# Optimization experiments

Hardware: AMD Instinct MI355X
Metric: run time of the kernel (lower is better)

The kernel has to match this reference:

```python
import jax, jax.numpy as jnp
import numpy as np

# Synthetic forest: T complete B-ary trees of depth D.
# Nodes stored level-major in `embeds`: level 0 (roots) first, then level 1, ...
# Level l has T*B**l nodes; children of node j at level l are rows j*B..j*B+B-1 of level l+1.
T_TREES, BRANCH, DEPTH = 16, 4, 8
IN_DIM, HIDDEN, N_LABEL = 128, 128, 5


def _level_layout():
    counts = [T_TREES * BRANCH ** l for l in range(DEPTH)]
    offsets = np.concatenate([[0], np.cumsum(counts)]).astype(np.int64)
    return counts, offsets


def setup_inputs() -> dict:
    key = jax.random.key(0)
    counts, offsets = _level_layout()
    n_total = int(offsets[-1])
    ks = jax.random.split(key, 16)
    s_in = 1.0 / np.sqrt(IN_DIM)
    s_h = 1.0 / np.sqrt(HIDDEN)
    d = {"embeds": jax.random.normal(ks[0], (n_total, IN_DIM), dtype=jnp.float32)}
    # gate params: *x linears have bias, *h linears are bias-free (as in torch module)
    d["Wix"] = jax.random.uniform(ks[1], (HIDDEN, IN_DIM), jnp.float32, -s_in, s_in)
    d["bix"] = jax.random.uniform(ks[2], (HIDDEN,), jnp.float32, -s_in, s_in)
    d["Wih"] = jax.random.uniform(ks[3], (HIDDEN, HIDDEN), jnp.float32, -s_h, s_h)
    d["Wfx"] = jax.random.uniform(ks[4], (HIDDEN, IN_DIM), jnp.float32, -s_in, s_in)
    d["bfx"] = jax.random.uniform(ks[5], (HIDDEN,), jnp.float32, -s_in, s_in)
    d["Wfh"] = jax.random.uniform(ks[6], (HIDDEN, HIDDEN), jnp.float32, -s_h, s_h)
    d["Wox"] = jax.random.uniform(ks[7], (HIDDEN, IN_DIM), jnp.float32, -s_in, s_in)
    d["box"] = jax.random.uniform(ks[8], (HIDDEN,), jnp.float32, -s_in, s_in)
    d["Woh"] = jax.random.uniform(ks[9], (HIDDEN, HIDDEN), jnp.float32, -s_h, s_h)
    d["Wux"] = jax.random.uniform(ks[10], (HIDDEN, IN_DIM), jnp.float32, -s_in, s_in)
    d["bux"] = jax.random.uniform(ks[11], (HIDDEN,), jnp.float32, -s_in, s_in)
    d["Wuh"] = jax.random.uniform(ks[12], (HIDDEN, HIDDEN), jnp.float32, -s_h, s_h)
    d["Wout"] = 0.01 * jax.random.normal(ks[13], (N_LABEL, HIDDEN), dtype=jnp.float32)
    d["bout"] = 0.01 * jax.random.normal(ks[14], (N_LABEL,), dtype=jnp.float32)
    return d


def reference(embeds, Wix, bix, Wih, Wfx, bfx, Wfh, Wox, box, Woh, Wux, bux, Wuh, Wout, bout):
    counts, offsets = _level_layout()
    H, B = HIDDEN, BRANCH
    child_h = child_c = None
    # leaves-first (level = DEPTH-1 .. 0), matching `while level >= 0` order
    for level in range(DEPTH - 1, -1, -1):
        n = counts[level]
        o = int(offsets[level])
        x = embeds[o:o + n]  # [n, in_dim] == index_select of this level's nodes
        if child_h is None:  # leaves: zero child state
            h_sum = jnp.zeros((n, H), embeds.dtype)
            fc_sum = jnp.zeros((n, H), embeds.dtype)
        else:
            # child-sum over the B children gathered from the previous level
            h_sum = child_h.reshape(n, B, H).sum(axis=1)  # child_h_sum
            fh = child_h @ Wfh.T  # [n*B, H]
            fx = jnp.repeat(x, B, axis=0) @ Wfx.T + bfx  # parent embed per child
            f = jax.nn.sigmoid(fx + fh)
            fc_sum = (f * child_c).reshape(n, B, H).sum(axis=1)  # child_fc_sum
        i = jax.nn.sigmoid(x @ Wix.T + bix + h_sum @ Wih.T)
        og = jax.nn.sigmoid(x @ Wox.T + box + h_sum @ Woh.T)
        u = jnp.tanh(x @ Wux.T + bux + h_sum @ Wuh.T)
        c = i * u + fc_sum
        h = og * jnp.tanh(c)
        child_c, child_h = c, h
    # output head at the root level (dropout is identity at eval)
    return child_h @ Wout.T + bout  # [T_TREES, N_LABEL]
```

## Files before the change

### kernel.cpp

```cpp
#include <hip/hip_runtime.h>
#include <hip/hip_bf16.h>


#define HID 128

typedef unsigned short u16;
typedef unsigned int u32;
typedef __attribute__((ext_vector_type(8))) short short8;
typedef __attribute__((ext_vector_type(4))) float floatx4;

__device__ __forceinline__ float bf2f(u16 u) {
  union { unsigned int u; float f; } v; v.u = ((unsigned int)u) << 16; return v.f;
}
__device__ __forceinline__ u16 f2bf(float f) {
  __hip_bfloat16 b = __float2bfloat16(f);
  return *reinterpret_cast<u16*>(&b);
}
__device__ __forceinline__ short8 f2bf8(float4 f0, float4 f1) {
  short8 s;
  s[0] = (short)f2bf(f0.x); s[1] = (short)f2bf(f0.y);
  s[2] = (short)f2bf(f0.z); s[3] = (short)f2bf(f0.w);
  s[4] = (short)f2bf(f1.x); s[5] = (short)f2bf(f1.y);
  s[6] = (short)f2bf(f1.z); s[7] = (short)f2bf(f1.w);
  return s;
}
__device__ __forceinline__ float sigm(float x) {
  return __builtin_amdgcn_rcpf(1.0f + __expf(-x));
}
__device__ __forceinline__ float tanh_fast(float x) {
  float ax = fabsf(x);
  float e = __expf(2.0f * ax);
  float t = 1.0f - 2.0f * __builtin_amdgcn_rcpf(e + 1.0f);
  return copysignf(t, x);
}

__global__ void prep_weights(const float* __restrict__ Wix, const float* __restrict__ Wih,
                             const float* __restrict__ Wfx, const float* __restrict__ Wfh,
                             const float* __restrict__ Wox, const float* __restrict__ Woh,
                             const float* __restrict__ Wux, const float* __restrict__ Wuh,
                             u16* __restrict__ Wcat, u16* __restrict__ Wfxb, u16* __restrict__ Wfhb)
{
  int t = blockIdx.x * 256 + threadIdx.x;
  if (t < 98304) {
    int nrow = t >> 8, k = t & 255;
    int gate = nrow >> 7, r = nrow & 127;
    float v;
    if (k < 128) {
      const float* W = (gate == 0) ? Wix : (gate == 1) ? Wox : Wux;
      v = W[r * 128 + k];
    } else {
      const float* W = (gate == 0) ? Wih : (gate == 1) ? Woh : Wuh;
      v = W[r * 128 + (k - 128)];
    }
    Wcat[t] = f2bf(v);
  } else if (t < 98304 + 16384) {
    int i = t - 98304;
    Wfxb[i] = f2bf(Wfx[i]);
  } else if (t < 98304 + 32768) {
    int i = t - 98304 - 16384;
    Wfhb[i] = f2bf(Wfh[i]);
  }
}

template <int MODE>
__global__ __launch_bounds__(512, 2)
void tree_kernel(const float* __restrict__ embeds,
                 const u16* __restrict__ Wcat,
                 const u16* __restrict__ Wfxb,
                 const u16* __restrict__ Wfhb,
                 const float* __restrict__ bix, const float* __restrict__ bfx,
                 const float* __restrict__ box, const float* __restrict__ bux,
                 u16* __restrict__ hf, float* __restrict__ fc_buf,
                 int n, int noff, int poff)
{
  constexpr bool HASC = (MODE >= 1);
  constexpr bool HASP = (MODE != 2);
  constexpr int OFF_SHS  = 16384;
  constexpr int OFF_SXP  = OFF_SHS + (HASC ? 16384 : 0);
  constexpr int OFF_SFXP = OFF_SXP + (HASP ? 4096 : 0);
  constexpr int SMEM_SZ  = OFF_SFXP + (HASP ? 16 * 132 * 4 : 0);
  __shared__ char smem[SMEM_SZ];
  u16*   sx   = (u16*)smem;
  u16*   shs  = (u16*)(smem + OFF_SHS);
  u16*   sxp  = (u16*)(smem + OFF_SXP);
  float* sfxp = (float*)(smem + OFF_SFXP);

  const int tid  = threadIdx.x;
  const int wave = tid >> 6;
  const int lane = tid & 63;
  const int lg   = lane >> 4;
  const int ln   = lane & 15;
  const int pbase = blockIdx.x * 64;
  const int col  = wave * 16 + ln;

  {
    int row = tid >> 3;
    int k0  = (tid & 7) * 16;
    const float* src = embeds + (size_t)(noff + pbase + row) * HID + k0;
    unsigned sw = ((unsigned)(row & 7)) << 4;
    char* dst = (char*)sx + row * 256;
    float4 f0 = *(const float4*)src;
    float4 f1 = *(const float4*)(src + 4);
    float4 f2 = *(const float4*)(src + 8);
    float4 f3 = *(const float4*)(src + 12);
    *(short8*)(dst + (((unsigned)(k0 * 2)) ^ sw))      = f2bf8(f0, f1);
    *(short8*)(dst + (((unsigned)(k0 * 2 + 16)) ^ sw)) = f2bf8(f2, f3);
  }
  if constexpr (HASC) {
    int row = tid >> 3, cg = tid & 7;
    const u16* src = hf + (size_t)(noff + pbase + row) * HID + cg * 16;
    short8 v0 = *(const short8*)src;
    short8 v1 = *(const short8*)(src + 8);
    unsigned sw = ((unsigned)(row & 7)) << 4;
    char* dst = (char*)shs + row * 256;
    *(short8*)(dst + ((cg * 32) ^ sw))      = v0;
    *(short8*)(dst + ((cg * 32 + 16) ^ sw)) = v1;
  }
  if constexpr (HASP) {
    if (tid < 128) {
      int row = tid >> 3;
      int k0  = (tid & 7) * 16;
      const float* src = embeds + (size_t)(poff + (pbase >> 2) + row) * HID + k0;
      unsigned sw = ((unsigned)(row & 7)) << 4;
      char* dst = (char*)sxp + row * 256;
      float4 f0 = *(const float4*)src;
      float4 f1 = *(const float4*)(src + 4);
      float4 f2 = *(const float4*)(src + 8);
      float4 f3 = *(const float4*)(src + 12);
      *(short8*)(dst + (((unsigned)(k0 * 2)) ^ sw))      = f2bf8(f0, f1);
      *(short8*)(dst + (((unsigned)(k0 * 2 + 16)) ^ sw)) = f2bf8(f2, f3);
    }
  }
  __syncthreads();

  float fcown[4][4];
  if constexpr (HASC) {
#pragma unroll
    for (int m = 0; m < 4; ++m)
#pragma unroll
      for (int r = 0; r < 4; ++r)
        fcown[m][r] = fc_buf[(size_t)(noff + pbase + m * 16 + lg * 4 + r) * HID + col];
  }

  floatx4 acc[4][3] = {};
  constexpr int KT = HASC ? 8 : 4;
#pragma unroll
  for (int kt = 0; kt < KT; ++kt) {
    short8 a[4];
#pragma unroll
    for (int m = 0; m < 4; ++m) {
      int row = m * 16 + ln;
      unsigned sw = ((unsigned)(row & 7)) << 4;
      const char* base = (kt < 4) ? (const char*)sx : (const char*)shs;
      int kb = ((kt & 3) * 32 + lg * 8) * 2;
      a[m] = *(const short8*)(base + row * 256 + (((unsigned)kb) ^ sw));
    }
#pragma unroll
    for (int g = 0; g < 3; ++g) {
      short8 b = *(const short8*)(Wcat + (size_t)((g * 8 + wave) * 16 + ln) * 256 + kt * 32 + lg * 8);
#pragma unroll
      for (int m = 0; m < 4; ++m)
        acc[m][g] = __builtin_amdgcn_mfma_f32_16x16x32_bf16(a[m], b, acc[m][g], 0, 0, 0);
    }
  }

  if constexpr (HASP) {
    floatx4 accxp = {};
#pragma unroll
    for (int kt = 0; kt < 4; ++kt) {
      short8 b = *(const short8*)(Wfxb + (size_t)(wave * 16 + ln) * HID + kt * 32 + lg * 8);
      unsigned sw = ((unsigned)(ln & 7)) << 4;
      short8 a = *(const short8*)((char*)sxp + ln * 256 +
                                  (((unsigned)((kt * 32 + lg * 8) * 2)) ^ sw));
      accxp = __builtin_amdgcn_mfma_f32_16x16x32_bf16(a, b, accxp, 0, 0, 0);
    }
#pragma unroll
    for (int r = 0; r < 4; ++r)
      sfxp[(lg * 4 + r) * 132 + col] = accxp[r];
  }
  __syncthreads();

  float cv[4][4];
  {
    float bi = bix[col], bo = box[col], bu = bux[col];
#pragma unroll
    for (int m = 0; m < 4; ++m) {
      float hs4 = 0.f;
#pragma unroll
      for (int r = 0; r < 4; ++r) {
        int row = m * 16 + lg * 4 + r;
        bool ok = (MODE == 2) ? (pbase + row < n) : true;
        if (ok) {
          float iv = sigm(acc[m][0][r] + bi);
          float ov = sigm(acc[m][1][r] + bo);
          float uv = tanh_fast(acc[m][2][r] + bu);
          float fcv = HASC ? fcown[m][r] : 0.f;
          float c = iv * uv + fcv;
          float hv = ov * tanh_fast(c);
          if constexpr (MODE == 2) {
            hf[(size_t)(noff + pbase + row) * HID + col] = f2bf(hv);
          } else {
            cv[m][r] = c;
            hs4 += hv;
            unsigned sw = ((unsigned)(row & 7)) << 4;
            *(u16*)((char*)sx + row * 256 + (((unsigned)(col * 2)) ^ sw)) = f2bf(hv);
          }
        }
      }
      if constexpr (HASP)
        hf[(size_t)(poff + (pbase >> 2) + m * 4 + lg) * HID + col] = f2bf(hs4);
    }
  }

  if constexpr (HASP) {
    __syncthreads();
    floatx4 ah[4] = {};
#pragma unroll
    for (int kt = 0; kt < 4; ++kt) {
      short8 b = *(const short8*)(Wfhb + (size_t)(wave * 16 + ln) * HID + kt * 32 + lg * 8);
#pragma unroll
      for (int m = 0; m < 4; ++m) {
        int row = m * 16 + ln;
        unsigned sw = ((unsigned)(row & 7)) << 4;
        short8 a = *(const short8*)((char*)sx + row * 256 +
                                    (((unsigned)((kt * 32 + lg * 8) * 2)) ^ sw));
        ah[m] = __builtin_amdgcn_mfma_f32_16x16x32_bf16(a, b, ah[m], 0, 0, 0);
      }
    }
    float bf = bfx[col];
#pragma unroll
    for (int m = 0; m < 4; ++m) {
      float fxv = sfxp[(m * 4 + lg) * 132 + col] + bf;
      float s = 0.f;
#pragma unroll
      for (int r = 0; r < 4; ++r)
        s += sigm(fxv + ah[m][r]) * cv[m][r];
      fc_buf[(size_t)(poff + (pbase >> 2) + m * 4 + lg) * HID + col] = s;
    }
  }
}

__global__ void out_kernel(const u16* __restrict__ hf, const float* __restrict__ Wout,
                           const float* __restrict__ bout, float* __restrict__ out)
{
  int t = threadIdx.x;
  if (t < 80) {
    int row = t / 5, lbl = t - row * 5;
    float s = bout[lbl];
    for (int k = 0; k < 128; ++k)
      s += bf2f(hf[row * 128 + k]) * Wout[lbl * 128 + k];
    out[t] = s;
  }
}

extern "C" void kernel_launch(void* const* d_in, const int* in_sizes, int n_in,
                              void* d_out, int out_size, void* d_ws, size_t ws_size,
                              hipStream_t stream)
{
  const float* embeds = (const float*)d_in[0];
  const float* Wix = (const float*)d_in[1];
  const float* bix = (const float*)d_in[2];
  const float* Wih = (const float*)d_in[3];
  const float* Wfx = (const float*)d_in[4];
  const float* bfx = (const float*)d_in[5];
  const float* Wfh = (const float*)d_in[6];
  const float* Wox = (const float*)d_in[7];
  const float* box = (const float*)d_in[8];
  const float* Woh = (const float*)d_in[9];
  const float* Wux = (const float*)d_in[10];
  const float* bux = (const float*)d_in[11];
  const float* Wuh = (const float*)d_in[12];
  const float* Wout = (const float*)d_in[13];
  const float* bout = (const float*)d_in[14];

  static const int counts[8]  = {16, 64, 256, 1024, 4096, 16384, 65536, 262144};
  static const int offsets[9] = {0, 16, 80, 336, 1360, 5456, 21840, 87376, 349520};

  char* ws = (char*)d_ws;
  u16*   hf     = (u16*)ws;
  float* fc_buf = (float*)(ws + 89477120);
  u16*   Wcat   = (u16*)(ws + 89477120 + 178954240);
  u16*   Wfxb   = Wcat + 384 * 256;
  u16*   Wfhb   = Wfxb + 128 * 128;

  prep_weights<<<512, 256, 0, stream>>>(Wix, Wih, Wfx, Wfh, Wox, Woh, Wux, Wuh,
                                        Wcat, Wfxb, Wfhb);

  tree_kernel<0><<<262144 / 64, 512, 0, stream>>>(
      embeds, Wcat, Wfxb, Wfhb, bix, bfx, box, bux,
      hf, fc_buf, 262144, 87376, 21840);

  for (int l = 6; l >= 1; --l) {
    int nl = counts[l];
    tree_kernel<1><<<nl / 64, 512, 0, stream>>>(
        embeds, Wcat, Wfxb, Wfhb, bix, bfx, box, bux,
        hf, fc_buf, nl, offsets[l], offsets[l - 1]);
  }

  tree_kernel<2><<<1, 512, 0, stream>>>(
      embeds, Wcat, Wfxb, Wfhb, bix, bfx, box, bux,
      hf, fc_buf, 16, 0, 0);

  out_kernel<<<1, 128, 0, stream>>>(hf, Wout, bout, (float*)d_out);
}
```

Before: 247.4 us.

## Fuse top tree levels and output head into one kernel; read parent embeds directly

Levels 2, 1 and 0 plus the output projection now run in a single persistent kernel with 4 blocks, each owning 4 root subtrees and looping over levels in shared memory. This removes four small kernel launches and their inter-kernel gaps. Separately, the parent-embedding forget-gate GEMM now reads fp32 embeds straight from global memory into MFMA operands instead of staging them in shared memory, which saves LDS space and a staging step. The fused tail uses only 4 blocks, so its per-level work is serialized within each block.

```diff
diff --git a/kernel.cpp b/kernel.cpp
--- a/kernel.cpp
+++ b/kernel.cpp
@@ -71,18 +71,15 @@
                  const float* __restrict__ bix, const float* __restrict__ bfx,
                  const float* __restrict__ box, const float* __restrict__ bux,
                  u16* __restrict__ hf, float* __restrict__ fc_buf,
-                 int n, int noff, int poff)
+                 int noff, int poff)
 {
   constexpr bool HASC = (MODE >= 1);
-  constexpr bool HASP = (MODE != 2);
   constexpr int OFF_SHS  = 16384;
-  constexpr int OFF_SXP  = OFF_SHS + (HASC ? 16384 : 0);
-  constexpr int OFF_SFXP = OFF_SXP + (HASP ? 4096 : 0);
-  constexpr int SMEM_SZ  = OFF_SFXP + (HASP ? 16 * 132 * 4 : 0);
+  constexpr int OFF_SFXP = OFF_SHS + (HASC ? 16384 : 0);
+  constexpr int SMEM_SZ  = OFF_SFXP + 16 * 132 * 4;
   __shared__ char smem[SMEM_SZ];
   u16*   sx   = (u16*)smem;
   u16*   shs  = (u16*)(smem + OFF_SHS);
-  u16*   sxp  = (u16*)(smem + OFF_SXP);
   float* sfxp = (float*)(smem + OFF_SFXP);
 
   const int tid  = threadIdx.x;
@@ -92,6 +89,7 @@
   const int ln   = lane & 15;
   const int pbase = blockIdx.x * 64;
   const int col  = wave * 16 + ln;
+  const int prow0 = poff + (pbase >> 2);
 
   {
     int row = tid >> 3;
@@ -116,13 +114,146 @@
     *(short8*)(dst + ((cg * 32) ^ sw))      = v0;
     *(short8*)(dst + ((cg * 32 + 16) ^ sw)) = v1;
   }
-  if constexpr (HASP) {
-    if (tid < 128) {
+  __syncthreads();
+
+  float fcown[4][4];
+  if constexpr (HASC) {
+#pragma unroll
+    for (int m = 0; m < 4; ++m)
+#pragma unroll
+      for (int r = 0; r < 4; ++r)
+        fcown[m][r] = fc_buf[(size_t)(noff + pbase + m * 16 + lg * 4 + r) * HID + col];
+  }
+
+  floatx4 acc[4][3] = {};
+  constexpr int KT = HASC ? 8 : 4;
+#pragma unroll
+  for (int kt = 0; kt < KT; ++kt) {
+    short8 a[4];
+#pragma unroll
+    for (int m = 0; m < 4; ++m) {
+      int row = m * 16 + ln;
+      unsigned sw = ((unsigned)(row & 7)) << 4;
+      const char* base = (kt < 4) ? (const char*)sx : (const char*)shs;
+      int kb = ((kt & 3) * 32 + lg * 8) * 2;
+      a[m] = *(const short8*)(base + row * 256 + (((unsigned)kb) ^ sw));
+    }
+#pragma unroll
+    for (int g = 0; g < 3; ++g) {
+      short8 b = *(const short8*)(Wcat + (size_t)((g * 8 + wave) * 16 + ln) * 256 + kt * 32 + lg * 8);
+#pragma unroll
+      for (int m = 0; m < 4; ++m)
+        acc[m][g] = __builtin_amdgcn_mfma_f32_16x16x32_bf16(a[m], b, acc[m][g], 0, 0, 0);
+    }
+  }
+
+  {
+    floatx4 accxp = {};
+    const float* xprow = embeds + (size_t)(prow0 + ln) * HID;
+#pragma unroll
+    for (int kt = 0; kt < 4; ++kt) {
+      short8 b = *(const short8*)(Wfxb + (size_t)(wave * 16 + ln) * HID + kt * 32 + lg * 8);
+      float4 f0 = *(const float4*)(xprow + kt * 32 + lg * 8);
+      float4 f1 = *(const float4*)(xprow + kt * 32 + lg * 8 + 4);
+      accxp = __builtin_amdgcn_mfma_f32_16x16x32_bf16(f2bf8(f0, f1), b, accxp, 0, 0, 0);
+    }
+#pragma unroll
+    for (int r = 0; r < 4; ++r)
+      sfxp[(lg * 4 + r) * 132 + col] = accxp[r];
+  }
+  __syncthreads();
+
+  float cv[4][4];
+  {
+    float bi = bix[col], bo = box[col], bu = bux[col];
+#pragma unroll
+    for (int m = 0; m < 4; ++m) {
+      float hs4 = 0.f;
+#pragma unroll
+      for (int r = 0; r < 4; ++r) {
+        int row = m * 16 + lg * 4 + r;
+        float iv = sigm(acc[m][0][r] + bi);
+        float ov = sigm(acc[m][1][r] + bo);
+        float uv = tanh_fast(acc[m][2][r] + bu);
+        float fcv = HASC ? fcown[m][r] : 0.f;
+        float c = iv * uv + fcv;
+        float hv = ov * tanh_fast(c);
+        cv[m][r] = c;
+        hs4 += hv;
+        unsigned sw = ((unsigned)(row & 7)) << 4;
+        *(u16*)((char*)sx + row * 256 + (((unsigned)(col * 2)) ^ sw)) = f2bf(hv);
+      }
+      hf[(size_t)(prow0 + m * 4 + lg) * HID + col] = f2bf(hs4);
+    }
+  }
+
+  {
+    __syncthreads();
+    floatx4 ah[4] = {};
+#pragma unroll
+    for (int kt = 0; kt < 4; ++kt) {
+      short8 b = *(const short8*)(Wfhb + (size_t)(wave * 16 + ln) * HID + kt * 32 + lg * 8);
+#pragma unroll
+      for (int m = 0; m < 4; ++m) {
+        int row = m * 16 + ln;
+        unsigned sw = ((unsigned)(row & 7)) << 4;
+        short8 a = *(const short8*)((char*)sx + row * 256 +
+                                    (((unsigned)((kt * 32 + lg * 8) * 2)) ^ sw));
+        ah[m] = __builtin_amdgcn_mfma_f32_16x16x32_bf16(a, b, ah[m], 0, 0, 0);
+      }
+    }
+    float bf = bfx[col];
+#pragma unroll
+    for (int m = 0; m < 4; ++m) {
+      float fxv = sfxp[(m * 4 + lg) * 132 + col] + bf;
+      float s = 0.f;
+#pragma unroll
+      for (int r = 0; r < 4; ++r)
+        s += sigm(fxv + ah[m][r]) * cv[m][r];
+      fc_buf[(size_t)(prow0 + m * 4 + lg) * HID + col] = s;
+    }
+  }
+}
+
+__global__ __launch_bounds__(512, 2)
+void fused_tail(const float* __restrict__ embeds,
+                const u16* __restrict__ Wcat,
+                const u16* __restrict__ Wfxb,
+                const u16* __restrict__ Wfhb,
+                const float* __restrict__ bix, const float* __restrict__ bfx,
+                const float* __restrict__ box, const float* __restrict__ bux,
+                const float* __restrict__ Wout, const float* __restrict__ bout,
+                u16* __restrict__ hf, float* __restrict__ fc_buf,
+                float* __restrict__ out)
+{
+  __shared__ char smem[16384 + 16384 + 16 * 132 * 4];
+  u16*   sx   = (u16*)smem;
+  u16*   shs  = (u16*)(smem + 16384);
+  float* sfxp = (float*)(smem + 32768);
+
+  const int tid  = threadIdx.x;
+  const int wave = tid >> 6;
+  const int lane = tid & 63;
+  const int lg   = lane >> 4;
+  const int ln   = lane & 15;
+  const int col  = wave * 16 + ln;
+  const int b    = blockIdx.x;
+
+  const int offs[3] = {0, 16, 80};
+
+#pragma unroll 1
+  for (int l = 2; l >= 0; --l) {
+    const int nrows = 64 >> (2 * (2 - l));
+    const int noff  = offs[l] + b * nrows;
+    const bool last = (l == 0);
+    const int poff  = last ? 0 : offs[l - 1] + b * (nrows >> 2);
+
+    {
       int row = tid >> 3;
       int k0  = (tid & 7) * 16;
-      const float* src = embeds + (size_t)(poff + (pbase >> 2) + row) * HID + k0;
+      const float* src = embeds + (size_t)(noff + row) * HID + k0;
       unsigned sw = ((unsigned)(row & 7)) << 4;
-      char* dst = (char*)sxp + row * 256;
+      char* dst = (char*)sx + row * 256;
       float4 f0 = *(const float4*)src;
       float4 f1 = *(const float4*)(src + 4);
       float4 f2 = *(const float4*)(src + 8);
@@ -130,126 +261,129 @@
       *(short8*)(dst + (((unsigned)(k0 * 2)) ^ sw))      = f2bf8(f0, f1);
       *(short8*)(dst + (((unsigned)(k0 * 2 + 16)) ^ sw)) = f2bf8(f2, f3);
     }
-  }
-  __syncthreads();
-
-  float fcown[4][4];
-  if constexpr (HASC) {
+    {
+      int row = tid >> 3, cg = tid & 7;
+      const u16* src = hf + (size_t)(noff + row) * HID + cg * 16;
+      short8 v0 = *(const short8*)src;
+      short8 v1 = *(const short8*)(src + 8);
+      unsigned sw = ((unsigned)(row & 7)) << 4;
+      char* dst = (char*)shs + row * 256;
+      *(short8*)(dst + ((cg * 32) ^ sw))      = v0;
+      *(short8*)(dst + ((cg * 32 + 16) ^ sw)) = v1;
+    }
+    __syncthreads();
+
+    float fcown[4][4];
 #pragma unroll
     for (int m = 0; m < 4; ++m)
 #pragma unroll
       for (int r = 0; r < 4; ++r)
-        fcown[m][r] = fc_buf[(size_t)(noff + pbase + m * 16 + lg * 4 + r) * HID + col];
-  }
-
-  floatx4 acc[4][3] = {};
-  constexpr int KT = HASC ? 8 : 4;
-#pragma unroll
-  for (int kt = 0; kt < KT; ++kt) {
-    short8 a[4];
-#pragma unroll
-    for (int m = 0; m < 4; ++m) {
-      int row = m * 16 + ln;
-      unsigned sw = ((unsigned)(row & 7)) << 4;
-      const char* base = (kt < 4) ? (const char*)sx : (const char*)shs;
-      int kb = ((kt & 3) * 32 + lg * 8) * 2;
-      a[m] = *(const short8*)(base + row * 256 + (((unsigned)kb) ^ sw));
-    }
-#pragma unroll
-    for (int g = 0; g < 3; ++g) {
-      short8 b = *(const short8*)(Wcat + (size_t)((g * 8 + wave) * 16 + ln) * 256 + kt * 32 + lg * 8);
-#pragma unroll
-      for (int m = 0; m < 4; ++m)
-        acc[m][g] = __builtin_amdgcn_mfma_f32_16x16x32_bf16(a[m], b, acc[m][g], 0, 0, 0);
-    }
-  }
-
-  if constexpr (HASP) {
-    floatx4 accxp = {};
-#pragma unroll
-    for (int kt = 0; kt < 4; ++kt) {
-      short8 b = *(const short8*)(Wfxb + (size_t)(wave * 16 + ln) * HID + kt * 32 + lg * 8);
-      unsigned sw = ((unsigned)(ln & 7)) << 4;
-      short8 a = *(const short8*)((char*)sxp + ln * 256 +
-                                  (((unsigned)((kt * 32 + lg * 8) * 2)) ^ sw));
-      accxp = __builtin_amdgcn_mfma_f32_16x16x32_bf16(a, b, accxp, 0, 0, 0);
-    }
-#pragma unroll
-    for (int r = 0; r < 4; ++r)
-      sfxp[(lg * 4 + r) * 132 + col] = accxp[r];
-  }
-  __syncthreads();
-
-  float cv[4][4];
-  {
-    float bi = bix[col], bo = box[col], bu = bux[col];
-#pragma unroll
-    for (int m = 0; m < 4; ++m) {
-      float hs4 = 0.f;
-#pragma unroll
-      for (int r = 0; r < 4; ++r) {
-        int row = m * 16 + lg * 4 + r;
-        bool ok = (MODE == 2) ? (pbase + row < n) : true;
-        if (ok) {
-          float iv = sigm(acc[m][0][r] + bi);
-          float ov = sigm(acc[m][1][r] + bo);
-          float uv = tanh_fast(acc[m][2][r] + bu);
-          float fcv = HASC ? fcown[m][r] : 0.f;
-          float c = iv * uv + fcv;
-          float hv = ov * tanh_fast(c);
-          if constexpr (MODE == 2) {
-            hf[(size_t)(noff + pbase + row) * HID + col] = f2bf(hv);
-          } else {
+        fcown[m][r] = fc_buf[(size_t)(noff + m * 16 + lg * 4 + r) * HID + col];
+
+    floatx4 acc[4][3] = {};
+#pragma unroll
+    for (int kt = 0; kt < 8; ++kt) {
+      short8 a[4];
+#pragma unroll
+      for (int m = 0; m < 4; ++m) {
+        int row = m * 16 + ln;
+        unsigned sw = ((unsigned)(row & 7)) << 4;
+        const char* base = (kt < 4) ? (const char*)sx : (const char*)shs;
+        int kb = ((kt & 3) * 32 + lg * 8) * 2;
+        a[m] = *(const short8*)(base + row * 256 + (((unsigned)kb) ^ sw));
+      }
+#pragma unroll
+      for (int g = 0; g < 3; ++g) {
+        short8 bb = *(const short8*)(Wcat + (size_t)((g * 8 + wave) * 16 + ln) * 256 + kt * 32 + lg * 8);
+#pragma unroll
+        for (int m = 0; m < 4; ++m)
+          acc[m][g] = __builtin_amdgcn_mfma_f32_16x16x32_bf16(a[m], bb, acc[m][g], 0, 0, 0);
+      }
+    }
+
+    if (!last) {
+      floatx4 accxp = {};
+      const float* xprow = embeds + (size_t)(poff + ln) * HID;
+#pragma unroll
+      for (int kt = 0; kt < 4; ++kt) {
+        short8 bb = *(const short8*)(Wfxb + (size_t)(wave * 16 + ln) * HID + kt * 32 + lg * 8);
+        float4 f0 = *(const float4*)(xprow + kt * 32 + lg * 8);
+        float4 f1 = *(const float4*)(xprow + kt * 32 + lg * 8 + 4);
+        accxp = __builtin_amdgcn_mfma_f32_16x16x32_bf16(f2bf8(f0, f1), bb, accxp, 0, 0, 0);
+      }
+#pragma unroll
+      for (int r = 0; r < 4; ++r)
+        sfxp[(lg * 4 + r) * 132 + col] = accxp[r];
+    }
+    __syncthreads();
+
+    float cv[4][4];
+    {
+      float bi = bix[col], bo = box[col], bu = bux[col];
+#pragma unroll
+      for (int m = 0; m < 4; ++m) {
+        float hs4 = 0.f;
+#pragma unroll
+        for (int r = 0; r < 4; ++r) {
+          int row = m * 16 + lg * 4 + r;
+          if (row < nrows) {
+            float iv = sigm(acc[m][0][r] + bi);
+            float ov = sigm(acc[m][1][r] + bo);
+            float uv = tanh_fast(acc[m][2][r] + bu);
+            float c = iv * uv + fcown[m][r];
+            float hv = ov * tanh_fast(c);
             cv[m][r] = c;
             hs4 += hv;
             unsigned sw = ((unsigned)(row & 7)) << 4;
             *(u16*)((char*)sx + row * 256 + (((unsigned)(col * 2)) ^ sw)) = f2bf(hv);
           }
         }
-      }
-      if constexpr (HASP)
-        hf[(size_t)(poff + (pbase >> 2) + m * 4 + lg) * HID + col] = f2bf(hs4);
-    }
-  }
-
-  if constexpr (HASP) {
+        if (!last && (m * 4 + lg) < (nrows >> 2))
+          hf[(size_t)(poff + m * 4 + lg) * HID + col] = f2bf(hs4);
+      }
+    }
+
+    if (!last) {
+      __syncthreads();
+      floatx4 ah[4] = {};
+#pragma unroll
+      for (int kt = 0; kt < 4; ++kt) {
+        short8 bb = *(const short8*)(Wfhb + (size_t)(wave * 16 + ln) * HID + kt * 32 + lg * 8);
+#pragma unroll
+        for (int m = 0; m < 4; ++m) {
+          int row = m * 16 + ln;
+          unsigned sw = ((unsigned)(row & 7)) << 4;
+          short8 a = *(const short8*)((char*)sx + row * 256 +
+                                      (((unsigned)((kt * 32 + lg * 8) * 2)) ^ sw));
+          ah[m] = __builtin_amdgcn_mfma_f32_16x16x32_bf16(a, bb, ah[m], 0, 0, 0);
+        }
+      }
+      float bf = bfx[col];
+#pragma unroll
+      for (int m = 0; m < 4; ++m) {
+        if ((m * 4 + lg) < (nrows >> 2)) {
+          float fxv = sfxp[(m * 4 + lg) * 132 + col] + bf;
+          float s = 0.f;
+#pragma unroll
+          for (int r = 0; r < 4; ++r)
+            s += sigm(fxv + ah[m][r]) * cv[m][r];
+          fc_buf[(size_t)(poff + m * 4 + lg) * HID + col] = s;
+        }
+      }
+    }
     __syncthreads();
-    floatx4 ah[4] = {};
-#pragma unroll
-    for (int kt = 0; kt < 4; ++kt) {
-      short8 b = *(const short8*)(Wfhb + (size_t)(wave * 16 + ln) * HID + kt * 32 + lg * 8);
-#pragma unroll
-      for (int m = 0; m < 4; ++m) {
-        int row = m * 16 + ln;
-        unsigned sw = ((unsigned)(row & 7)) << 4;
-        short8 a = *(const short8*)((char*)sx + row * 256 +
-                                    (((unsigned)((kt * 32 + lg * 8) * 2)) ^ sw));
-        ah[m] = __builtin_amdgcn_mfma_f32_16x16x32_bf16(a, b, ah[m], 0, 0, 0);
-      }
-    }
-    float bf = bfx[col];
-#pragma unroll
-    for (int m = 0; m < 4; ++m) {
-      float fxv = sfxp[(m * 4 + lg) * 132 + col] + bf;
-      float s = 0.f;
-#pragma unroll
-      for (int r = 0; r < 4; ++r)
-        s += sigm(fxv + ah[m][r]) * cv[m][r];
-      fc_buf[(size_t)(poff + (pbase >> 2) + m * 4 + lg) * HID + col] = s;
-    }
-  }
-}
-
-__global__ void out_kernel(const u16* __restrict__ hf, const float* __restrict__ Wout,
-                           const float* __restrict__ bout, float* __restrict__ out)
-{
-  int t = threadIdx.x;
-  if (t < 80) {
-    int row = t / 5, lbl = t - row * 5;
+  }
+
+  if (tid < 20) {
+    int r = tid / 5, lbl = tid - r * 5;
+    unsigned sw = ((unsigned)r) << 4;
     float s = bout[lbl];
+    const float* wr = Wout + lbl * 128;
+    const char* hrow = (const char*)sx + r * 256;
+#pragma unroll 4
     for (int k = 0; k < 128; ++k)
-      s += bf2f(hf[row * 128 + k]) * Wout[lbl * 128 + k];
-    out[t] = s;
+      s += bf2f(*(const u16*)(hrow + (((unsigned)(k * 2)) ^ sw))) * wr[k];
+    out[(4 * b + r) * 5 + lbl] = s;
   }
 }
 
@@ -288,18 +422,16 @@
 
   tree_kernel<0><<<262144 / 64, 512, 0, stream>>>(
       embeds, Wcat, Wfxb, Wfhb, bix, bfx, box, bux,
-      hf, fc_buf, 262144, 87376, 21840);
-
-  for (int l = 6; l >= 1; --l) {
+      hf, fc_buf, 87376, 21840);
+
+  for (int l = 6; l >= 3; --l) {
     int nl = counts[l];
     tree_kernel<1><<<nl / 64, 512, 0, stream>>>(
         embeds, Wcat, Wfxb, Wfhb, bix, bfx, box, bux,
-        hf, fc_buf, nl, offsets[l], offsets[l - 1]);
-  }
-
-  tree_kernel<2><<<1, 512, 0, stream>>>(
+        hf, fc_buf, offsets[l], offsets[l - 1]);
+  }
+
+  fused_tail<<<4, 512, 0, stream>>>(
       embeds, Wcat, Wfxb, Wfhb, bix, bfx, box, bux,
-      hf, fc_buf, 16, 0, 0);
-
-  out_kernel<<<1, 128, 0, stream>>>(hf, Wout, bout, (float*)d_out);
-}
+      Wout, bout, hf, fc_buf, (float*)d_out);
+}
```

Result: slower. 274.1 us (+10.8%).
